# Kernel optimization log

Measured on AMD Instinct MI355X. Metric: run time of the kernel, lower is better.

Reference implementation:

```python
import jax, jax.numpy as jnp
import numpy as np

IN_CHANNELS = 64


def _haar_weights(in_channels: int) -> jnp.ndarray:
    # Matches torch construction: (4, 1, 2, 2), then sign flips, *0.25, tiled per channel.
    w = np.ones((4, 1, 2, 2), dtype=np.float32)
    w[1, 0, 0, 1] = -1
    w[1, 0, 1, 1] = -1
    w[2, 0, 1, 0] = -1
    w[2, 0, 1, 1] = -1
    w[3, 0, 1, 0] = -1
    w[3, 0, 0, 1] = -1
    w = w * 0.25
    w = np.concatenate([w] * in_channels, axis=0)  # (4*C, 1, 2, 2) OIHW
    return jnp.asarray(w)


def setup_inputs() -> dict:
    key = jax.random.key(0)
    B, C, H, W = 8, IN_CHANNELS, 512, 512
    inputs = jax.random.normal(key, (B, C, H, W), dtype=jnp.float32)
    weights = _haar_weights(IN_CHANNELS)
    return {"inputs": inputs, "weights": weights}


def reference(inputs, weights):
    # Forward Haar transform (reverse=False path).
    B, C, H, W = inputs.shape
    # Depthwise (grouped) 2x2 stride-2 conv: out channels = 4*C, grouped by C.
    out = jax.lax.conv_general_dilated(
        inputs, weights,
        window_strides=(2, 2), padding='VALID',
        dimension_numbers=('NCHW', 'OIHW', 'NCHW'),
        feature_group_count=C,
    )  # (B, 4*C, H/2, W/2), channel-major layout [c0:(LL,LH,HL,HH), c1:...]
    # Regroup to subband-major: (B, 4, C, h, w) -> (B, 4*C, h, w)
    h, w = H // 2, W // 2
    out = out.reshape(B, C, 4, h, w).transpose(0, 2, 1, 3, 4).reshape(B, C * 4, h, w)
    return out
```

## Files before the change

kernel.cpp:

```cpp
#include <hip/hip_runtime.h>


constexpr int B  = 8;
constexpr int C  = 64;
constexpr int H  = 512;
constexpr int W  = 512;
constexpr int HO = H / 2;
constexpr int WO = W / 2;
constexpr int W4 = WO / 4;

typedef float f32x4 __attribute__((ext_vector_type(4)));

__global__ __launch_bounds__(256) void haar_fwd(const float* __restrict__ x,
                                                float* __restrict__ y) {
    const int total = B * C * HO * W4;
    int idx = blockIdx.x * blockDim.x + threadIdx.x;
    if (idx >= total) return;

    const int j4 = idx & (W4 - 1);
    const int i  = (idx >> 6) & (HO - 1);
    const int m  = idx >> 14;

    const float* r0 = x + ((size_t)m * H + 2 * (size_t)i) * W + 8 * (size_t)j4;
    const float* r1 = r0 + W;
    const f32x4 r0a = __builtin_nontemporal_load(reinterpret_cast<const f32x4*>(r0));
    const f32x4 r0b = __builtin_nontemporal_load(reinterpret_cast<const f32x4*>(r0 + 4));
    const f32x4 r1a = __builtin_nontemporal_load(reinterpret_cast<const f32x4*>(r1));
    const f32x4 r1b = __builtin_nontemporal_load(reinterpret_cast<const f32x4*>(r1 + 4));

    const float a0 = r0a.x, b0 = r0a.y, a1 = r0a.z, b1 = r0a.w;
    const float a2 = r0b.x, b2 = r0b.y, a3 = r0b.z, b3 = r0b.w;
    const float c0 = r1a.x, d0 = r1a.y, c1 = r1a.z, d1 = r1a.w;
    const float c2 = r1b.x, d2 = r1b.y, c3 = r1b.z, d3 = r1b.w;

    f32x4 ll, k1, k2, k3;
    ll.x = 0.25f * (a0 + b0 + c0 + d0);
    ll.y = 0.25f * (a1 + b1 + c1 + d1);
    ll.z = 0.25f * (a2 + b2 + c2 + d2);
    ll.w = 0.25f * (a3 + b3 + c3 + d3);

    k1.x = 0.25f * (a0 - b0 + c0 - d0);
    k1.y = 0.25f * (a1 - b1 + c1 - d1);
    k1.z = 0.25f * (a2 - b2 + c2 - d2);
    k1.w = 0.25f * (a3 - b3 + c3 - d3);

    k2.x = 0.25f * (a0 + b0 - c0 - d0);
    k2.y = 0.25f * (a1 + b1 - c1 - d1);
    k2.z = 0.25f * (a2 + b2 - c2 - d2);
    k2.w = 0.25f * (a3 + b3 - c3 - d3);

    k3.x = 0.25f * (a0 - b0 - c0 + d0);
    k3.y = 0.25f * (a1 - b1 - c1 + d1);
    k3.z = 0.25f * (a2 - b2 - c2 + d2);
    k3.w = 0.25f * (a3 - b3 - c3 + d3);

    const size_t plane  = (size_t)HO * WO;
    const size_t rowoff = (size_t)i * WO + 4 * (size_t)j4;
    float* yb = y + ((size_t)(m >> 6) * 4 * C + (m & (C - 1))) * plane + rowoff;

    __builtin_nontemporal_store(ll, reinterpret_cast<f32x4*>(yb));
    __builtin_nontemporal_store(k1, reinterpret_cast<f32x4*>(yb + (size_t)C * plane));
    __builtin_nontemporal_store(k2, reinterpret_cast<f32x4*>(yb + (size_t)2 * C * plane));
    __builtin_nontemporal_store(k3, reinterpret_cast<f32x4*>(yb + (size_t)3 * C * plane));
}

extern "C" void kernel_launch(void* const* d_in, const int* in_sizes, int n_in,
                              void* d_out, int out_size, void* d_ws, size_t ws_size,
                              hipStream_t stream) {
    const float* x = (const float*)d_in[0];
    float* y = (float*)d_out;

    const int total = B * C * HO * W4;
    const int threads = 256;
    const int blocks = (total + threads - 1) / threads;
    haar_fwd<<<blocks, threads, 0, stream>>>(x, y);
}
```

Measured before the change: 192.1 us.

## Stage input rows through LDS for fully contiguous coalesced global loads

```diff
diff --git a/kernel.cpp b/kernel.cpp
--- a/kernel.cpp
+++ b/kernel.cpp
@@ -7,26 +7,43 @@
 constexpr int W  = 512;
 constexpr int HO = H / 2;
 constexpr int WO = W / 2;
-constexpr int W4 = WO / 4;
+constexpr int RPB  = 4;
+constexpr int ROWS = 2 * RPB;
+constexpr int CHUNKS = ROWS * W / 4;
 
 typedef float f32x4 __attribute__((ext_vector_type(4)));
 
 __global__ __launch_bounds__(256) void haar_fwd(const float* __restrict__ x,
                                                 float* __restrict__ y) {
-    const int total = B * C * HO * W4;
-    int idx = blockIdx.x * blockDim.x + threadIdx.x;
-    if (idx >= total) return;
+    __shared__ float lds[ROWS * W];
 
-    const int j4 = idx & (W4 - 1);
-    const int i  = (idx >> 6) & (HO - 1);
-    const int m  = idx >> 14;
+    const int t  = threadIdx.x;
+    const int ig = blockIdx.x & 63;
+    const int m  = blockIdx.x >> 6;
 
-    const float* r0 = x + ((size_t)m * H + 2 * (size_t)i) * W + 8 * (size_t)j4;
-    const float* r1 = r0 + W;
-    const f32x4 r0a = __builtin_nontemporal_load(reinterpret_cast<const f32x4*>(r0));
-    const f32x4 r0b = __builtin_nontemporal_load(reinterpret_cast<const f32x4*>(r0 + 4));
-    const f32x4 r1a = __builtin_nontemporal_load(reinterpret_cast<const f32x4*>(r1));
-    const f32x4 r1b = __builtin_nontemporal_load(reinterpret_cast<const f32x4*>(r1 + 4));
+    const float* src = x + ((size_t)m * H + (size_t)ig * ROWS) * W;
+
+    #pragma unroll
+    for (int k = 0; k < 4; ++k) {
+        const int ch  = t + k * 256;
+        const f32x4 v = __builtin_nontemporal_load(
+            reinterpret_cast<const f32x4*>(src + 4 * (size_t)ch));
+        const int row = ch >> 7;
+        const int c   = ch & 127;
+        const int pos = (c >> 1) + ((c & 1) << 6);
+        *reinterpret_cast<f32x4*>(&lds[row * W + 4 * pos]) = v;
+    }
+    __syncthreads();
+
+    const int j4 = t & 63;
+    const int rp = t >> 6;
+
+    const float* l0 = &lds[(2 * rp) * W];
+    const float* l1 = l0 + W;
+    const f32x4 r0a = *reinterpret_cast<const f32x4*>(l0 + 4 * j4);
+    const f32x4 r0b = *reinterpret_cast<const f32x4*>(l0 + 4 * (64 + j4));
+    const f32x4 r1a = *reinterpret_cast<const f32x4*>(l1 + 4 * j4);
+    const f32x4 r1b = *reinterpret_cast<const f32x4*>(l1 + 4 * (64 + j4));
 
     const float a0 = r0a.x, b0 = r0a.y, a1 = r0a.z, b1 = r0a.w;
     const float a2 = r0b.x, b2 = r0b.y, a3 = r0b.z, b3 = r0b.w;
@@ -54,6 +71,7 @@
     k3.z = 0.25f * (a2 - b2 - c2 + d2);
     k3.w = 0.25f * (a3 - b3 - c3 + d3);
 
+    const int i = ig * RPB + rp;
     const size_t plane  = (size_t)HO * WO;
     const size_t rowoff = (size_t)i * WO + 4 * (size_t)j4;
     float* yb = y + ((size_t)(m >> 6) * 4 * C + (m & (C - 1))) * plane + rowoff;
@@ -70,8 +88,6 @@
     const float* x = (const float*)d_in[0];
     float* y = (float*)d_out;
 
-    const int total = B * C * HO * W4;
-    const int threads = 256;
-    const int blocks = (total + threads - 1) / threads;
-    haar_fwd<<<blocks, threads, 0, stream>>>(x, y);
+    const int blocks = B * C * (HO / RPB);
+    haar_fwd<<<blocks, 256, 0, stream>>>(x, y);
 }
```

After: 213.0 us. 10.9% more time.
